# Performance work log

Measured on AMD Instinct MI355X. Metric: run time of the kernel, lower is better.

The kernel has to match this reference:

```python
import jax, jax.numpy as jnp
import numpy as np


def setup_inputs() -> dict:
    key = jax.random.key(0)
    k1, k2 = jax.random.split(key)
    B, V = 256, 128000
    logits = jax.random.normal(k1, (B, V), dtype=jnp.float32)
    temperatures = jax.random.uniform(k2, (B,), dtype=jnp.float32, minval=0.0, maxval=1.5)
    # make a quarter of the sequences greedy (temperature == 0) to exercise both paths
    temperatures = temperatures.at[: B // 4].set(0.0)
    return {"logits": logits, "temperatures": temperatures}


def reference(logits, temperatures):
    # Temperature-scaled logits; temperature==0 rows use temp 1 for the (unused) sampling path.
    logits = logits.astype(jnp.float32)
    safe_t = jnp.where(temperatures == 0, jnp.ones_like(temperatures), temperatures)
    scaled = logits / safe_t[:, None]  # [B, V]

    # probs (same math as torch.softmax(scaled, -1)); materialized for faithfulness
    probs = jax.nn.softmax(scaled, axis=-1)

    greedy_tokens = jnp.argmax(logits, axis=-1)  # [B]

    # torch.multinomial(probs, 1) == Gumbel-max / categorical over scaled logits
    sample_key = jax.random.key(42)
    sampled_tokens = jax.random.categorical(sample_key, scaled, axis=-1)  # [B]

    return jnp.where(temperatures == 0, greedy_tokens, sampled_tokens)
```

## Files before the change

### kernel.cpp

```cpp
#include <hip/hip_runtime.h>
#include <stdint.h>

namespace {

constexpr int kB = 256;
constexpr int kV = 128000;
constexpr int kSplit = 8;
constexpr int kBlk = 256;
constexpr int kChunk = kV / kSplit;

struct Part { float val; int idx; };

__device__ __forceinline__ uint32_t rotl32(uint32_t x, int r) {
  return (x << r) | (x >> (32 - r));
}

__device__ __forceinline__ uint32_t threefry_bits(uint32_t x1) {
  constexpr uint32_t ks0 = 0u;
  constexpr uint32_t ks1 = 42u;
  constexpr uint32_t ks2 = 0x1BD11BDAu ^ ks0 ^ ks1;
  uint32_t x0 = ks0;
  x1 += ks1;
#define TF_ROUND(r) { x0 += x1; x1 = rotl32(x1, r); x1 ^= x0; }
  TF_ROUND(13) TF_ROUND(15) TF_ROUND(26) TF_ROUND(6)
  x0 += ks1; x1 += ks2 + 1u;
  TF_ROUND(17) TF_ROUND(29) TF_ROUND(16) TF_ROUND(24)
  x0 += ks2; x1 += ks0 + 2u;
  TF_ROUND(13) TF_ROUND(15) TF_ROUND(26) TF_ROUND(6)
  x0 += ks0; x1 += ks1 + 3u;
  TF_ROUND(17) TF_ROUND(29) TF_ROUND(16) TF_ROUND(24)
  x0 += ks1; x1 += ks2 + 4u;
  TF_ROUND(13) TF_ROUND(15) TF_ROUND(26) TF_ROUND(6)
  x0 += ks2; x1 += ks0 + 5u;
#undef TF_ROUND
  return x0 ^ x1;
}

__device__ __forceinline__ float gumbel_from_bits(uint32_t bits) {
  constexpr float kTiny = 1.17549435e-38f;
  constexpr float kNegLn2 = -0.69314718055994530942f;
  float f = __uint_as_float((bits >> 9) | 0x3F800000u) - 1.0f;
  float u = fmaxf(kTiny, f + kTiny);
  float y = __builtin_amdgcn_logf(u) * kNegLn2;
  return __builtin_amdgcn_logf(y) * kNegLn2;
}

__global__ __launch_bounds__(kBlk) void sampler_partial(
    const float* __restrict__ logits, const float* __restrict__ temps,
    Part* __restrict__ parts) {
  const int r = blockIdx.x / kSplit;
  const int g = blockIdx.x % kSplit;
  const float t = temps[r];
  const bool greedy = (t == 0.0f);
  const int start = g * kChunk;
  const int end = start + kChunk;
  const float* __restrict__ row = logits + (size_t)r * kV;

  float best = -__builtin_inff();
  int bi = 0;

  if (greedy) {
    for (int v = start + (int)threadIdx.x * 4; v + 3 < end; v += kBlk * 4) {
      float4 a = *reinterpret_cast<const float4*>(row + v);
      float la[4] = {a.x, a.y, a.z, a.w};
#pragma unroll
      for (int j = 0; j < 4; ++j) {
        if (la[j] > best) { best = la[j]; bi = v + j; }
      }
    }
  } else {
    for (int v = start + (int)threadIdx.x * 4; v + 3 < end; v += kBlk * 4) {
      float4 a = *reinterpret_cast<const float4*>(row + v);
      float la[4] = {a.x, a.y, a.z, a.w};
      const uint32_t base = (uint32_t)(r * kV + v);
#pragma unroll
      for (int j = 0; j < 4; ++j) {
        float gb = gumbel_from_bits(threefry_bits(base + (uint32_t)j));
        float key = fmaf(t, gb, la[j]);
        if (key > best) { best = key; bi = v + j; }
      }
    }
  }

  __shared__ float sv[kBlk];
  __shared__ int si[kBlk];
  sv[threadIdx.x] = best;
  si[threadIdx.x] = bi;
  __syncthreads();
  for (int s = kBlk / 2; s > 0; s >>= 1) {
    if ((int)threadIdx.x < s) {
      float ov = sv[threadIdx.x + s]; int oi = si[threadIdx.x + s];
      float mv = sv[threadIdx.x];     int mi = si[threadIdx.x];
      if (ov > mv || (ov == mv && oi < mi)) {
        sv[threadIdx.x] = ov; si[threadIdx.x] = oi;
      }
    }
    __syncthreads();
  }
  if (threadIdx.x == 0) {
    parts[r * kSplit + g].val = sv[0];
    parts[r * kSplit + g].idx = si[0];
  }
}

__global__ __launch_bounds__(kB) void sampler_final(
    const Part* __restrict__ parts, int* __restrict__ out) {
  const int r = threadIdx.x;
  if (r < kB) {
    float bv = -__builtin_inff();
    int bi = 0;
    for (int g = 0; g < kSplit; ++g) {
      Part p = parts[r * kSplit + g];
      if (p.val > bv || (p.val == bv && p.idx < bi)) { bv = p.val; bi = p.idx; }
    }
    out[r] = bi;
  }
}

}

extern "C" void kernel_launch(void* const* d_in, const int* in_sizes, int n_in,
                              void* d_out, int out_size, void* d_ws, size_t ws_size,
                              hipStream_t stream) {
  const float* logits = (const float*)d_in[0];
  const float* temps = (const float*)d_in[1];
  int* out = (int*)d_out;
  Part* parts = (Part*)d_ws;

  sampler_partial<<<dim3(kB * kSplit), dim3(kBlk), 0, stream>>>(logits, temps, parts);
  sampler_final<<<dim3(1), dim3(kB), 0, stream>>>(parts, out);
}
```

Baseline: 204.4 us.

## Prefetch all row loads up front and raise split to 25 blocks per row

Raises the per-row split from 8 to 25 so each block handles 5120 elements, exactly 5 float4 loads per thread. All loads are issued into registers before the compute loop, giving more memory-level parallelism and more blocks across the GPU. It also uses a builtin rotate in threefry and drops the fmaxf clamp in the Gumbel transform. If the chunk is not a multiple of 1024 the tail would be lost, but 5120 divides evenly here.

Result: slower. 208.9 us (+2.2%).

```diff
diff --git a/kernel.cpp b/kernel.cpp
--- a/kernel.cpp
+++ b/kernel.cpp
@@ -5,15 +5,12 @@
 
 constexpr int kB = 256;
 constexpr int kV = 128000;
-constexpr int kSplit = 8;
+constexpr int kSplit = 25;
 constexpr int kBlk = 256;
 constexpr int kChunk = kV / kSplit;
+constexpr int kIter = kChunk / (kBlk * 4);
 
 struct Part { float val; int idx; };
-
-__device__ __forceinline__ uint32_t rotl32(uint32_t x, int r) {
-  return (x << r) | (x >> (32 - r));
-}
 
 __device__ __forceinline__ uint32_t threefry_bits(uint32_t x1) {
   constexpr uint32_t ks0 = 0u;
@@ -21,7 +18,7 @@
   constexpr uint32_t ks2 = 0x1BD11BDAu ^ ks0 ^ ks1;
   uint32_t x0 = ks0;
   x1 += ks1;
-#define TF_ROUND(r) { x0 += x1; x1 = rotl32(x1, r); x1 ^= x0; }
+#define TF_ROUND(r) { x0 += x1; x1 = __builtin_rotateleft32(x1, r); x1 ^= x0; }
   TF_ROUND(13) TF_ROUND(15) TF_ROUND(26) TF_ROUND(6)
   x0 += ks1; x1 += ks2 + 1u;
   TF_ROUND(17) TF_ROUND(29) TF_ROUND(16) TF_ROUND(24)
@@ -40,7 +37,7 @@
   constexpr float kTiny = 1.17549435e-38f;
   constexpr float kNegLn2 = -0.69314718055994530942f;
   float f = __uint_as_float((bits >> 9) | 0x3F800000u) - 1.0f;
-  float u = fmaxf(kTiny, f + kTiny);
+  float u = f + kTiny;
   float y = __builtin_amdgcn_logf(u) * kNegLn2;
   return __builtin_amdgcn_logf(y) * kNegLn2;
 }
@@ -51,28 +48,35 @@
   const int r = blockIdx.x / kSplit;
   const int g = blockIdx.x % kSplit;
   const float t = temps[r];
-  const bool greedy = (t == 0.0f);
   const int start = g * kChunk;
-  const int end = start + kChunk;
   const float* __restrict__ row = logits + (size_t)r * kV;
+  const int tbase = start + (int)threadIdx.x * 4;
+
+  float4 a[kIter];
+#pragma unroll
+  for (int it = 0; it < kIter; ++it) {
+    a[it] = *reinterpret_cast<const float4*>(row + tbase + it * kBlk * 4);
+  }
 
   float best = -__builtin_inff();
   int bi = 0;
 
-  if (greedy) {
-    for (int v = start + (int)threadIdx.x * 4; v + 3 < end; v += kBlk * 4) {
-      float4 a = *reinterpret_cast<const float4*>(row + v);
-      float la[4] = {a.x, a.y, a.z, a.w};
+  if (t == 0.0f) {
+#pragma unroll
+    for (int it = 0; it < kIter; ++it) {
+      const int v = tbase + it * kBlk * 4;
+      float la[4] = {a[it].x, a[it].y, a[it].z, a[it].w};
 #pragma unroll
       for (int j = 0; j < 4; ++j) {
         if (la[j] > best) { best = la[j]; bi = v + j; }
       }
     }
   } else {
-    for (int v = start + (int)threadIdx.x * 4; v + 3 < end; v += kBlk * 4) {
-      float4 a = *reinterpret_cast<const float4*>(row + v);
-      float la[4] = {a.x, a.y, a.z, a.w};
+#pragma unroll
+    for (int it = 0; it < kIter; ++it) {
+      const int v = tbase + it * kBlk * 4;
       const uint32_t base = (uint32_t)(r * kV + v);
+      float la[4] = {a[it].x, a[it].y, a[it].z, a[it].w};
 #pragma unroll
       for (int j = 0; j < 4; ++j) {
         float gb = gumbel_from_bits(threefry_bits(base + (uint32_t)j));
@@ -109,6 +113,7 @@
   if (r < kB) {
     float bv = -__builtin_inff();
     int bi = 0;
+#pragma unroll
     for (int g = 0; g < kSplit; ++g) {
       Part p = parts[r * kSplit + g];
       if (p.val > bv || (p.val == bv && p.idx < bi)) { bv = p.val; bi = p.idx; }
```
